# Optimization experiments

Hardware: AMD Instinct MI355X
Metric: run time of the kernel (lower is better)

Reference implementation:

```python
import jax, jax.numpy as jnp
import numpy as np

QMAX = 255.0  # bit=8 unsigned activation range


def ste_round(x):
    # straight-through round: exact integer rounding in fwd, identity grad
    return x + jax.lax.stop_gradient(jnp.round(x) - x)


def conv3x3(x, w, stride=1):
    return jax.lax.conv_general_dilated(
        x, w, window_strides=(stride, stride), padding=((1, 1), (1, 1)),
        dimension_numbers=('NCHW', 'OIHW', 'NCHW'))


def setup_inputs() -> dict:
    key = jax.random.key(0)
    k0, k1, k2 = jax.random.split(key, 3)
    N, C, H, W = 64, 256, 28, 28
    # uint8 activations and int8 (symmetric) weights, stored as integer-valued fp32
    x = jax.random.randint(k0, (N, C, H, W), 0, 256).astype(jnp.float32)
    w1 = jax.random.randint(k1, (C, C, 3, 3), -128, 128).astype(jnp.float32)
    w2 = jax.random.randint(k2, (C, C, 3, 3), -128, 128).astype(jnp.float32)
    f = jnp.float32
    return dict(
        x=x, w1=w1, w2=w2,
        s_x=f(0.05), z_x=f(128.0),
        s_w1=f(0.01), s_conv1=f(0.08), z_conv1=f(120.0),
        s_w2=f(0.01), s_conv2=f(0.07), z_conv2=f(130.0),
        s_add=f(0.09), z_add=f(125.0))


def qconv(x_q, w_q, s_in, z_in, s_w, s_out, z_out, stride=1):
    # integer-arithmetic conv: sum((x - z_in) * w) then requantize
    acc = conv3x3(x_q - z_in, w_q, stride)
    M = s_in * s_w / s_out  # per-cluster requant multiplier (cluster 0)
    return jnp.clip(ste_round(M * acc) + z_out, 0.0, QMAX)


def qadd(a, s_a, z_a, b, s_b, z_b, s_out, z_out):
    # fused dequant of both branches + residual add + requant
    y = (s_a / s_out) * (a - z_a) + (s_b / s_out) * (b - z_b)
    return jnp.clip(ste_round(y) + z_out, 0.0, QMAX)


def reference(x, w1, w2, s_x, z_x, s_w1, s_conv1, z_conv1,
              s_w2, s_conv2, z_conv2, s_add, z_add):
    out = qconv(x, w1, s_x, z_x, s_w1, s_conv1, z_conv1)          # conv1
    out = qconv(out, w2, s_conv1, z_conv1, s_w2, s_conv2, z_conv2)  # conv2
    return qadd(x, s_x, z_x, out, s_conv2, z_conv2, s_add, z_add)   # shortcut
```

## Files before the change

kernel.cpp:

```cpp
#include <hip/hip_runtime.h>
#include <stdint.h>

#define HWP 784
#define NPOS 50176
#define PLN ((size_t)NPOS * 64)
#define SLAB_ROWS 186
#define NCHUNK 2976
#define PAD_OFF 47616

typedef int   int4v   __attribute__((ext_vector_type(4)));
typedef int   int16v  __attribute__((ext_vector_type(16)));
typedef float float4v __attribute__((ext_vector_type(4)));
using as1_cv = const __attribute__((address_space(1))) void;
using as3_v  = __attribute__((address_space(3))) void;

__global__ __launch_bounds__(256) void k_prep(const float* __restrict__ x,
                                              int8_t* __restrict__ x8,
                                              const float* __restrict__ wa,
                                              const float* __restrict__ wb,
                                              int8_t* __restrict__ w8a,
                                              int8_t* __restrict__ w8b,
                                              int* __restrict__ wsa,
                                              int* __restrict__ wsb) {
    __shared__ __align__(16) int8_t smem[30592];
    const int tid = threadIdx.x;
    if (blockIdx.x < 896) {
        int* lA = (int*)smem;
        int* lB = (int*)(smem + 15360);
        const int P0 = blockIdx.x * 56;
        const int n = P0 / HWP;
        const int hw0 = P0 % HWP;
        const float* xb = x + (size_t)n * 256 * HWP + hw0;
#pragma unroll
        for (int k = 0; k < 14; ++k) {
            int e = tid + k * 256;
            int c = e / 14, pq = e % 14;
            float4v v = *(const float4v*)(xb + (size_t)c * HWP + pq * 4);
            int b0 = ((int)v[0] - 128) & 255;
            int b1 = ((int)v[1] - 128) & 255;
            int b2 = ((int)v[2] - 128) & 255;
            int b3 = ((int)v[3] - 128) & 255;
            lA[c * 15 + pq] = b0 | (b1 << 8) | (b2 << 16) | (b3 << 24);
        }
        __syncthreads();
#pragma unroll
        for (int k = 0; k < 4; ++k) {
            int u = tid + k * 256;
            if (u < 896) {
                int cg = u / 14, pq = u % 14;
                int d0 = lA[(cg * 4 + 0) * 15 + pq];
                int d1 = lA[(cg * 4 + 1) * 15 + pq];
                int d2 = lA[(cg * 4 + 2) * 15 + pq];
                int d3 = lA[(cg * 4 + 3) * 15 + pq];
#pragma unroll
                for (int j = 0; j < 4; ++j) {
                    int sh = j * 8;
                    int o = ((d0 >> sh) & 255) | (((d1 >> sh) & 255) << 8)
                          | (((d2 >> sh) & 255) << 16) | (((d3 >> sh) & 255) << 24);
                    lB[(pq * 4 + j) * 68 + cg] = o;
                }
            }
        }
        __syncthreads();
#pragma unroll
        for (int k = 0; k < 4; ++k) {
            int ch = tid + k * 256;
            if (ch < 896) {
                int g = ch / 224, rem = ch % 224;
                int pos = rem >> 2, c4 = rem & 3;
                int4v val = *(const int4v*)&lB[pos * 68 + g * 16 + c4 * 4];
                *(int4v*)(x8 + (size_t)g * PLN + (size_t)(P0 + pos) * 64 + c4 * 16) = val;
            }
        }
    } else {
        int8_t* lds8 = smem;
        int* red = (int*)(smem + 2304);
        const int bid2 = blockIdx.x - 896;
        const int which = bid2 >> 8;
        const int oc = bid2 & 255;
        const float* w = which ? wb : wa;
        int8_t* w8 = which ? w8b : w8a;
        int* wsum = which ? wsb : wsa;
        const float* src = w + (size_t)oc * 2304;
        const int g = oc >> 5;
        const int lbase = oc & 31;
        int acc = 0;
#pragma unroll
        for (int k = 0; k < 9; ++k) {
            int m = k * 256 + tid;
            int v = (int)src[m];
            acc += v;
            int ic = m / 9, tap = m % 9;
            int kb = ic >> 6, s2 = (ic >> 5) & 1, hi = (ic >> 4) & 1, j = ic & 15;
            lds8[((tap * 4 + kb) * 2 + s2) * 32 + hi * 16 + j] = (int8_t)v;
        }
        red[tid] = acc;
        __syncthreads();
        if (tid < 144) {
            int c = tid >> 1, hi = tid & 1;
            int4v val = *(const int4v*)&lds8[c * 32 + hi * 16];
            size_t oo = ((size_t)(c * 8 + g) * 64 + hi * 32 + lbase) * 16;
            *(int4v*)(w8 + oo) = val;
        }
        for (int st = 128; st > 0; st >>= 1) {
            if (tid < st) red[tid] += red[tid + st];
            __syncthreads();
        }
        if (tid == 0) wsum[oc] = red[0];
    }
}

template<bool FUSED>
__global__ __launch_bounds__(256, 2) void k_qconv_t(const int8_t* __restrict__ in8,
        const int8_t* __restrict__ w8, const int* __restrict__ wsum,
        const float* __restrict__ s_in_p, const float* __restrict__ s_w_p,
        const float* __restrict__ s_out_p, const float* __restrict__ z_in_p,
        const float* __restrict__ z_out_p, int8_t* __restrict__ out8,
        const int8_t* __restrict__ x8, const float* __restrict__ sxp,
        const float* __restrict__ zxp, const float* __restrict__ sap,
        const float* __restrict__ zap, float* __restrict__ outf) {
    __shared__ __align__(16) int8_t slab[47872];
    const int tid = threadIdx.x;
    const int lane = tid & 63;
    const int half = lane >> 5;
    const int wv = tid >> 6;
    const int bid = blockIdx.x;
    const int tile = (bid & 7) * 49 + (bid >> 3);
    const int p0 = tile * 128;
    const int plane = wv;

#pragma unroll
    for (int k = 0; k < 12; ++k) {
        int chunkid = tid + k * 256;
        if (chunkid < NCHUNK) {
            int q = chunkid >> 4;
            int cs = chunkid & 15;
            int cg = cs ^ (q & 15);
            int qg = p0 - 29 + q;
            qg = qg < 0 ? 0 : (qg > NPOS - 1 ? NPOS - 1 : qg);
            const int8_t* src = in8 + (size_t)(cg >> 2) * PLN
                                    + (size_t)qg * 64 + (cg & 3) * 16;
            __builtin_amdgcn_global_load_lds((as1_cv*)src,
                                             (as3_v*)&slab[chunkid * 16], 16, 0, 0);
        }
    }

    const int zi = (int)z_in_p[0] - 128;
    const int spl = (zi & 0xff) * 0x01010101;
    if (tid < 16) {
        int4v pv; pv[0] = spl; pv[1] = spl; pv[2] = spl; pv[3] = spl;
        *(int4v*)&slab[PAD_OFF + tid * 16] = pv;
    }

    int rowpos[4], ph[4], pw[4];
#pragma unroll
    for (int mt = 0; mt < 4; ++mt) {
        rowpos[mt] = mt * 32 + (lane & 31);
        int p = p0 + rowpos[mt];
        int hw = p % HWP;
        ph[mt] = hw / 28;
        pw[mt] = hw % 28;
    }

    int16v acc[4][2];
#pragma unroll
    for (int mt = 0; mt < 4; ++mt)
#pragma unroll
        for (int nt = 0; nt < 2; ++nt)
#pragma unroll
            for (int r = 0; r < 16; ++r) acc[mt][nt][r] = 0;

    const int8_t* wlane = w8 + plane * 2048 + lane * 16;

    __syncthreads();

    int4v bc00 = *(const int4v*)(wlane);
    int4v bc10 = *(const int4v*)(wlane + 1024);
    int4v bc01 = *(const int4v*)(wlane + 8192);
    int4v bc11 = *(const int4v*)(wlane + 9216);

#pragma unroll
    for (int u = 0; u < 36; ++u) {
        const int tap = u >> 2, kb = u & 3;
        const int dh = tap / 3 - 1;
        const int dw = tap % 3 - 1;
        int4v bn00, bn10, bn01, bn11;
        if (u < 35) {
            const int8_t* wb_ = wlane + (size_t)(u + 1) * 16384;
            bn00 = *(const int4v*)(wb_);
            bn10 = *(const int4v*)(wb_ + 1024);
            bn01 = *(const int4v*)(wb_ + 8192);
            bn11 = *(const int4v*)(wb_ + 9216);
        }
        int4v a[4][2];
#pragma unroll
        for (int mt = 0; mt < 4; ++mt) {
            int q = rowpos[mt] + dh * 28 + dw + 29;
            bool ok = ((unsigned)(ph[mt] + dh) < 28u) & ((unsigned)(pw[mt] + dw) < 28u);
            int ab = (ok ? (q << 8) : PAD_OFF) ^ ((q & 15) << 4) ^ (half << 4);
            a[mt][0] = *(const int4v*)&slab[ab ^ ((kb * 4 + 0) << 4)];
            a[mt][1] = *(const int4v*)&slab[ab ^ ((kb * 4 + 2) << 4)];
        }
#pragma unroll
        for (int mt = 0; mt < 4; ++mt) {
            acc[mt][0] = __builtin_amdgcn_mfma_i32_32x32x32_i8(a[mt][0], bc00,
                                                               acc[mt][0], 0, 0, 0);
            acc[mt][1] = __builtin_amdgcn_mfma_i32_32x32x32_i8(a[mt][0], bc10,
                                                               acc[mt][1], 0, 0, 0);
        }
#pragma unroll
        for (int mt = 0; mt < 4; ++mt) {
            acc[mt][0] = __builtin_amdgcn_mfma_i32_32x32x32_i8(a[mt][1], bc01,
                                                               acc[mt][0], 0, 0, 0);
            acc[mt][1] = __builtin_amdgcn_mfma_i32_32x32x32_i8(a[mt][1], bc11,
                                                               acc[mt][1], 0, 0, 0);
        }
        bc00 = bn00; bc10 = bn10; bc01 = bn01; bc11 = bn11;
    }

    const float Mf = s_in_p[0] * s_w_p[0] / s_out_p[0];
    const float zof = z_out_p[0];
    const int zoffi = 128 - (int)z_in_p[0];

    if (!FUSED) {
        __syncthreads();
        int8_t* tpb = slab + wv * 10240;
#pragma unroll
        for (int mt = 0; mt < 4; ++mt)
#pragma unroll
            for (int nt = 0; nt < 2; ++nt) {
                int oc = plane * 64 + nt * 32 + (lane & 31);
                int corr = zoffi * wsum[oc];
#pragma unroll
                for (int r = 0; r < 16; ++r) {
                    int prow = (r & 3) + 8 * (r >> 2) + 4 * half;
                    int pl = mt * 32 + prow;
                    float q = rintf(Mf * (float)(acc[mt][nt][r] + corr)) + zof;
                    q = fminf(fmaxf(q, 0.0f), 255.0f);
                    tpb[pl * 80 + nt * 32 + (lane & 31)] = (int8_t)((int)q - 128);
                }
            }
#pragma unroll
        for (int h2 = 0; h2 < 2; ++h2) {
            const int rr = h2 * 64 + lane;
            int8_t* o8p = out8 + (size_t)plane * PLN + (size_t)(p0 + rr) * 64;
            const int8_t* rowp = tpb + rr * 80;
#pragma unroll
            for (int k = 0; k < 4; ++k)
                *(int4v*)(o8p + k * 16) = *(const int4v*)(rowp + k * 16);
        }
    } else {
        const float ra = sxp[0] / sap[0];
        const float rb = s_out_p[0] / sap[0];
        const float zx = zxp[0];
        const float z2 = z_out_p[0];
        const float za = zap[0];
        __syncthreads();
        float* tp = (float*)slab + wv * 2080;
        const int pl = lane & 31;
#pragma unroll
        for (int mt = 0; mt < 4; ++mt) {
#pragma unroll
            for (int nt = 0; nt < 2; ++nt) {
                int oc = plane * 64 + nt * 32 + (lane & 31);
                int corr = zoffi * wsum[oc];
#pragma unroll
                for (int r = 0; r < 16; ++r) {
                    int prow = (r & 3) + 8 * (r >> 2) + 4 * half;
                    float q2 = rintf(Mf * (float)(acc[mt][nt][r] + corr)) + zof;
                    q2 = fminf(fmaxf(q2, 0.0f), 255.0f);
                    tp[prow * 65 + nt * 32 + (lane & 31)] = q2;
                }
            }
            const int pglob = p0 + mt * 32 + pl;
            const int n = pglob / HWP;
            const int hwo = pglob % HWP;
            const int8_t* x8p = x8 + (size_t)plane * PLN + (size_t)pglob * 64 + half * 32;
            int4v r0 = *(const int4v*)x8p;
            int4v r1 = *(const int4v*)(x8p + 16);
            int xb[8];
            xb[0] = r0[0]; xb[1] = r0[1]; xb[2] = r0[2]; xb[3] = r0[3];
            xb[4] = r1[0]; xb[5] = r1[1]; xb[6] = r1[2]; xb[7] = r1[3];
            float* obase = outf + ((size_t)(n * 256 + plane * 64 + half * 32)) * HWP + hwo;
#pragma unroll
            for (int j = 0; j < 32; ++j) {
                int bv = (xb[j >> 2] >> ((j & 3) * 8)) & 255;
                int xval = (int)(int8_t)bv + 128;
                float q2 = tp[pl * 65 + half * 32 + j];
                float y = ra * ((float)xval - zx) + rb * (q2 - z2);
                float qf = rintf(y) + za;
                qf = fminf(fmaxf(qf, 0.0f), 255.0f);
                obase[(size_t)j * HWP] = qf;
            }
        }
    }
}

extern "C" void kernel_launch(void* const* d_in, const int* in_sizes, int n_in,
                              void* d_out, int out_size, void* d_ws, size_t ws_size,
                              hipStream_t stream) {
    (void)in_sizes; (void)n_in; (void)out_size; (void)ws_size;
    const float* x    = (const float*)d_in[0];
    const float* w1   = (const float*)d_in[1];
    const float* w2   = (const float*)d_in[2];
    const float* s_x  = (const float*)d_in[3];
    const float* z_x  = (const float*)d_in[4];
    const float* s_w1 = (const float*)d_in[5];
    const float* s_c1 = (const float*)d_in[6];
    const float* z_c1 = (const float*)d_in[7];
    const float* s_w2 = (const float*)d_in[8];
    const float* s_c2 = (const float*)d_in[9];
    const float* z_c2 = (const float*)d_in[10];
    const float* s_ad = (const float*)d_in[11];
    const float* z_ad = (const float*)d_in[12];
    float* out = (float*)d_out;

    int8_t* ws    = (int8_t*)d_ws;
    int8_t* x8    = ws;
    int8_t* o1    = ws + 12845056;
    int8_t* w8a   = ws + 25690112;
    int8_t* w8b   = ws + 26279936;
    int*    wsum1 = (int*)(ws + 26869760);
    int*    wsum2 = (int*)(ws + 26870784);

    k_prep<<<1408, 256, 0, stream>>>(x, x8, w1, w2, w8a, w8b, wsum1, wsum2);
    k_qconv_t<false><<<392, 256, 0, stream>>>(x8, w8a, wsum1,
        s_x, s_w1, s_c1, z_x, z_c1, o1,
        nullptr, nullptr, nullptr, nullptr, nullptr, nullptr);
    k_qconv_t<true><<<392, 256, 0, stream>>>(o1, w8b, wsum2,
        s_c1, s_w2, s_c2, z_c1, z_c2, nullptr,
        x8, s_x, z_x, s_ad, z_ad, out);
}
```

Before: 196.6 us.

## Software-pipeline LDS A-fragment loads and interleave with MFMAs via sched_group_barrier

Restructures the 36-step int8 MFMA inner loop so the LDS reads of the next A fragment are issued while the current MFMA half-batch executes. It keeps a double buffer (a_cur/a_nxt) and computes the next tap's slab address early. sched_group_barrier hints interleave the DS reads, global weight loads and MFMAs. The aim is to hide LDS latency behind matrix work, at the cost of more live registers and a risk of spills or lower occupancy.

```diff
diff --git a/kernel.cpp b/kernel.cpp
--- a/kernel.cpp
+++ b/kernel.cpp
@@ -13,6 +13,9 @@
 typedef float float4v __attribute__((ext_vector_type(4)));
 using as1_cv = const __attribute__((address_space(1))) void;
 using as3_v  = __attribute__((address_space(3))) void;
+
+#define SGB __builtin_amdgcn_sched_group_barrier
+#define MFMA_I8 __builtin_amdgcn_mfma_i32_32x32x32_i8
 
 __global__ __launch_bounds__(256) void k_prep(const float* __restrict__ x,
                                               int8_t* __restrict__ x8,
@@ -179,11 +182,25 @@
     int4v bc01 = *(const int4v*)(wlane + 8192);
     int4v bc11 = *(const int4v*)(wlane + 9216);
 
+    int ab[4];
+#pragma unroll
+    for (int mt = 0; mt < 4; ++mt) {
+        int q = rowpos[mt];
+        bool ok = ((unsigned)(ph[mt] - 1) < 28u) & ((unsigned)(pw[mt] - 1) < 28u);
+        ab[mt] = (ok ? (q << 8) : PAD_OFF) ^ ((q & 15) << 4) ^ (half << 4);
+    }
+    int4v a_cur[4], a_nxt[4];
+#pragma unroll
+    for (int mt = 0; mt < 4; ++mt)
+        a_cur[mt] = *(const int4v*)&slab[ab[mt]];
+
 #pragma unroll
     for (int u = 0; u < 36; ++u) {
-        const int tap = u >> 2, kb = u & 3;
-        const int dh = tap / 3 - 1;
-        const int dw = tap % 3 - 1;
+        const int kb = u & 3;
+        const int koff1 = (kb * 4 + 2) << 4;
+#pragma unroll
+        for (int mt = 0; mt < 4; ++mt)
+            a_nxt[mt] = *(const int4v*)&slab[ab[mt] ^ koff1];
         int4v bn00, bn10, bn01, bn11;
         if (u < 35) {
             const int8_t* wb_ = wlane + (size_t)(u + 1) * 16384;
@@ -192,30 +209,44 @@
             bn01 = *(const int4v*)(wb_ + 8192);
             bn11 = *(const int4v*)(wb_ + 9216);
         }
-        int4v a[4][2];
 #pragma unroll
         for (int mt = 0; mt < 4; ++mt) {
-            int q = rowpos[mt] + dh * 28 + dw + 29;
-            bool ok = ((unsigned)(ph[mt] + dh) < 28u) & ((unsigned)(pw[mt] + dw) < 28u);
-            int ab = (ok ? (q << 8) : PAD_OFF) ^ ((q & 15) << 4) ^ (half << 4);
-            a[mt][0] = *(const int4v*)&slab[ab ^ ((kb * 4 + 0) << 4)];
-            a[mt][1] = *(const int4v*)&slab[ab ^ ((kb * 4 + 2) << 4)];
+            acc[mt][0] = MFMA_I8(a_cur[mt], bc00, acc[mt][0], 0, 0, 0);
+            acc[mt][1] = MFMA_I8(a_cur[mt], bc10, acc[mt][1], 0, 0, 0);
+        }
+        SGB(0x100, 4, 0);
+        if (u < 35) SGB(0x020, 4, 0);
+        SGB(0x008, 8, 0);
+#pragma unroll
+        for (int mt = 0; mt < 4; ++mt) a_cur[mt] = a_nxt[mt];
+
+        if (u < 35) {
+            const int un = u + 1;
+            const int tapn = un >> 2, kbn = un & 3;
+            const int dhn = tapn / 3 - 1;
+            const int dwn = tapn % 3 - 1;
+            const int koff0 = (kbn * 4) << 4;
+#pragma unroll
+            for (int mt = 0; mt < 4; ++mt) {
+                int q = rowpos[mt] + dhn * 28 + dwn + 29;
+                bool ok = ((unsigned)(ph[mt] + dhn) < 28u)
+                        & ((unsigned)(pw[mt] + dwn) < 28u);
+                ab[mt] = (ok ? (q << 8) : PAD_OFF) ^ ((q & 15) << 4) ^ (half << 4);
+                a_nxt[mt] = *(const int4v*)&slab[ab[mt] ^ koff0];
+            }
         }
 #pragma unroll
         for (int mt = 0; mt < 4; ++mt) {
-            acc[mt][0] = __builtin_amdgcn_mfma_i32_32x32x32_i8(a[mt][0], bc00,
-                                                               acc[mt][0], 0, 0, 0);
-            acc[mt][1] = __builtin_amdgcn_mfma_i32_32x32x32_i8(a[mt][0], bc10,
-                                                               acc[mt][1], 0, 0, 0);
-        }
-#pragma unroll
-        for (int mt = 0; mt < 4; ++mt) {
-            acc[mt][0] = __builtin_amdgcn_mfma_i32_32x32x32_i8(a[mt][1], bc01,
-                                                               acc[mt][0], 0, 0, 0);
-            acc[mt][1] = __builtin_amdgcn_mfma_i32_32x32x32_i8(a[mt][1], bc11,
-                                                               acc[mt][1], 0, 0, 0);
-        }
-        bc00 = bn00; bc10 = bn10; bc01 = bn01; bc11 = bn11;
+            acc[mt][0] = MFMA_I8(a_cur[mt], bc01, acc[mt][0], 0, 0, 0);
+            acc[mt][1] = MFMA_I8(a_cur[mt], bc11, acc[mt][1], 0, 0, 0);
+        }
+        if (u < 35) SGB(0x100, 4, 0);
+        SGB(0x008, 8, 0);
+        if (u < 35) {
+#pragma unroll
+            for (int mt = 0; mt < 4; ++mt) a_cur[mt] = a_nxt[mt];
+            bc00 = bn00; bc10 = bn10; bc01 = bn01; bc11 = bn11;
+        }
     }
 
     const float Mf = s_in_p[0] * s_w_p[0] / s_out_p[0];
```

Measured after the change: 197.4 us. No clear change (+0.4%).
